# Kernel optimization log

Hardware: AMD Instinct MI355X
Metric: run time of the kernel (lower is better)

The kernel has to match this reference:

```python
import jax, jax.numpy as jnp
import numpy as np

N_NODES = 50000
N_EDGES = 800000
NODE_F = 128
EDGE_F = 64
HID = 128
N_LAYERS = 3
BN_EPS = 1e-5


def _bn(x, g, b):
    # BatchNorm1d in training mode: per-feature batch mean/var (biased)
    m = jnp.mean(x, axis=0)
    v = jnp.mean(jnp.square(x - m), axis=0)
    return g * (x - m) * jax.lax.rsqrt(v + BN_EPS) + b


def _gelu(x):
    return jax.nn.gelu(x, approximate=False)


def setup_inputs() -> dict:
    key = jax.random.key(0)
    ks = jax.random.split(key, 16)
    s_in = 1.0 / np.sqrt(NODE_F)
    s_h = 1.0 / np.sqrt(HID)
    s_2h = 1.0 / np.sqrt(2 * HID)
    s_e = 1.0 / np.sqrt(EDGE_F)
    L = N_LAYERS
    inp = {
        "x": jax.random.normal(ks[0], (N_NODES, NODE_F), jnp.float32),
        "edge_index": jax.random.randint(ks[1], (2, N_EDGES), 0, N_NODES, jnp.int64),
        "edge_attr": jax.random.normal(ks[2], (N_EDGES, EDGE_F), jnp.float32),
        # node_embed: Linear + BN
        "emb_w": jax.random.uniform(ks[3], (NODE_F, HID), jnp.float32, -s_in, s_in),
        "emb_b": jnp.zeros((HID,), jnp.float32),
        "emb_g": jnp.ones((HID,), jnp.float32),
        "emb_beta": jnp.zeros((HID,), jnp.float32),
        # per-layer GINEConv params (stacked over layers)
        "eps": jnp.zeros((L,), jnp.float32),
        "lin_e_w": jax.random.uniform(ks[4], (L, EDGE_F, HID), jnp.float32, -s_e, s_e),
        "lin_e_b": jnp.zeros((L, HID), jnp.float32),
        "w1": jax.random.uniform(ks[5], (L, HID, 2 * HID), jnp.float32, -s_h, s_h),
        "b1": jnp.zeros((L, 2 * HID), jnp.float32),
        "g1": jnp.ones((L, 2 * HID), jnp.float32),
        "beta1": jnp.zeros((L, 2 * HID), jnp.float32),
        "w2": jax.random.uniform(ks[6], (L, 2 * HID, HID), jnp.float32, -s_2h, s_2h),
        "b2": jnp.zeros((L, HID), jnp.float32),
        "g2": jnp.ones((L, HID), jnp.float32),
        "beta2": jnp.zeros((L, HID), jnp.float32),
    }
    return inp


def reference(x, edge_index, edge_attr, emb_w, emb_b, emb_g, emb_beta,
              eps, lin_e_w, lin_e_b, w1, b1, g1, beta1, w2, b2, g2, beta2):
    src = edge_index[0]  # source nodes j
    dst = edge_index[1]  # target nodes i
    n = x.shape[0]

    h = _gelu(_bn(x @ emb_w + emb_b, emb_g, emb_beta))  # [N, H]
    intermediates = [h]
    for i in range(N_LAYERS):
        e = edge_attr @ lin_e_w[i] + lin_e_b[i]          # [E, H]
        msg = jax.nn.relu(h[src] + e)                    # gather + fuse + relu
        agg = jax.ops.segment_sum(msg, dst, num_segments=n)  # scatter-add
        z = (1.0 + eps[i]) * h + agg
        z = _gelu(_bn(z @ w1[i] + b1[i], g1[i], beta1[i]))
        h = _gelu(_bn(z @ w2[i] + b2[i], g2[i], beta2[i]))
        intermediates.append(h)
    return jnp.concatenate(intermediates, axis=-1)  # [N, (L+1)*H]
```

## Files before the change

### kernel.cpp

```cpp
#include <hip/hip_runtime.h>
#include <hip/hip_bf16.h>

typedef __hip_bfloat16 bf16;
typedef __attribute__((ext_vector_type(8))) short bf16x8;
typedef __attribute__((ext_vector_type(4))) float f32x4;

#define HIDDEN 128
#define NNODES 50000
#define NEDGES 800000

static __device__ __forceinline__ float b2f(bf16 v) { return __bfloat162float(v); }
static __device__ __forceinline__ short f2bs(float f) {
    bf16 b = __float2bfloat16(f);
    return *reinterpret_cast<const short*>(&b);
}
static __device__ __forceinline__ float bs2f(short s) {
    unsigned x = ((unsigned)(unsigned short)s) << 16;
    return *reinterpret_cast<const float*>(&x);
}
static __device__ __forceinline__ bf16x8 ld_frag(const bf16* p) {
    return *reinterpret_cast<const bf16x8*>(p);
}
static __device__ __forceinline__ bf16x8 zero8() {
    bf16x8 z = {0, 0, 0, 0, 0, 0, 0, 0};
    return z;
}
static __device__ __forceinline__ float u2f_lo(unsigned u) {
    unsigned x = u << 16; return *reinterpret_cast<const float*>(&x);
}
static __device__ __forceinline__ float u2f_hi(unsigned u) {
    unsigned x = u & 0xffff0000u; return *reinterpret_cast<const float*>(&x);
}
static __device__ __forceinline__ bf16x8 ld_a8(const void* base, size_t off, bool f32) {
    if (!f32) return *reinterpret_cast<const bf16x8*>((const bf16*)base + off);
    const float4* p = reinterpret_cast<const float4*>((const float*)base + off);
    float4 u = p[0], w = p[1];
    bf16x8 r;
    r[0]=f2bs(u.x); r[1]=f2bs(u.y); r[2]=f2bs(u.z); r[3]=f2bs(u.w);
    r[4]=f2bs(w.x); r[5]=f2bs(w.y); r[6]=f2bs(w.z); r[7]=f2bs(w.w);
    return r;
}
static __device__ __forceinline__ float gelu_ex(float v) {
    return 0.5f * v * (1.f + erff(v * 0.70710678118654752f));
}

#define C_EMB_B   0
#define C_EMB_G   128
#define C_EMB_BT  256
#define C_EPS     384
#define C_LIN_B   400
#define C_B1      800
#define C_G1      1568
#define C_BT1     2336
#define C_B2      3104
#define C_G2      3488
#define C_BT2     3872

__global__ void k_init(float* __restrict__ stats, int* __restrict__ cursorA,
                       int* __restrict__ cursorB, int doSort) {
    int tid = blockIdx.x * 256 + threadIdx.x;
    int stride = gridDim.x * 256;
    for (int i = tid; i < 3584; i += stride) stats[i] = 0.f;
    if (doSort) for (int i = tid; i < NNODES; i += stride) cursorA[i] = 0;
    for (int i = tid; i < NNODES; i += stride) cursorB[i] = 0;
}

__global__ void k_detect_cvt(const unsigned* __restrict__ gones,
                             const unsigned* __restrict__ eiw, int* __restrict__ flags,
                             const void* emb_b, const void* emb_g, const void* emb_bt,
                             const void* eps, const void* lin_b, const void* b1,
                             const void* g1, const void* bt1, const void* b2,
                             const void* g2, const void* bt2, bf16* __restrict__ canon) {
    __shared__ int sf;
    if (threadIdx.x == 0) {
        int f0 = (gones[0] == 0x3F803F80u) ? 1 : 0;
        unsigned s = 0;
        for (int i = 1; i < 64; i += 2) s |= eiw[i];
        flags[0] = f0; flags[1] = (s == 0u) ? 1 : 0;
        sf = f0;
    }
    __syncthreads();
    bool f32 = (sf == 0);
    const void* ps[11] = {emb_b, emb_g, emb_bt, eps, lin_b, b1, g1, bt1, b2, g2, bt2};
    const int   ns[11] = {128, 128, 128, 3, 384, 768, 768, 768, 384, 384, 384};
    const int   os[11] = {C_EMB_B, C_EMB_G, C_EMB_BT, C_EPS, C_LIN_B, C_B1,
                          C_G1, C_BT1, C_B2, C_G2, C_BT2};
    for (int seg = 0; seg < 11; ++seg)
        for (int i = threadIdx.x; i < ns[seg]; i += 256) {
            short v = f32 ? f2bs(((const float*)ps[seg])[i]) : ((const short*)ps[seg])[i];
            ((short*)canon)[os[seg] + i] = v;
        }
}

__global__ void k_repack_all(const void* __restrict__ emb_w, const void* __restrict__ lin_w,
                             const void* __restrict__ w1, const void* __restrict__ w2,
                             bf16* __restrict__ Wf, const int* __restrict__ flags) {
    const int starts[11] = {0, 16384, 24576, 32768, 40960, 73728, 106496,
                            139264, 172032, 204800, 237568};
    int idx = blockIdx.x * 256 + threadIdx.x;
    if (idx >= 237568) return;
    bool f32 = (flags[0] == 0);
    int seg = 0;
    while (idx >= starts[seg + 1]) ++seg;
    int local = idx - starts[seg];
    const void* base; long long eoff; int K, N;
    if (seg == 0)      { base = emb_w; eoff = 0;                          K = 128; N = 128; }
    else if (seg <= 3) { base = lin_w; eoff = (long long)(seg - 1) * 8192;  K = 64;  N = 128; }
    else if (seg <= 6) { base = w1;    eoff = (long long)(seg - 4) * 32768; K = 128; N = 256; }
    else               { base = w2;    eoff = (long long)(seg - 7) * 32768; K = 256; N = 128; }
    int j    = local & 7;
    int lane = (local >> 3) & 63;
    int rest = local >> 9;
    int NF   = N >> 4;
    int ks   = rest / NF;
    int nf   = rest - ks * NF;
    int k = ks * 32 + ((lane >> 4) << 3) + j;
    int n = (nf << 4) + (lane & 15);
    long long src = eoff + (long long)k * N + n;
    short v = f32 ? f2bs(((const float*)base)[src]) : ((const short*)base)[src];
    ((short*)Wf)[idx] = v;
}

__global__ void k_hist(const void* __restrict__ ei, int* __restrict__ deg,
                       const int* __restrict__ flags) {
    bool i64 = (flags[1] == 1);
    for (int e = blockIdx.x * 256 + threadIdx.x; e < NEDGES; e += gridDim.x * 256) {
        int d = i64 ? (int)((const long long*)ei)[NEDGES + e] : ((const int*)ei)[NEDGES + e];
        if ((unsigned)d < NNODES) atomicAdd(&deg[d], 1);
    }
}

__global__ __launch_bounds__(1024) void k_scan(const int* __restrict__ deg,
                                               int* __restrict__ rowptr) {
    __shared__ int part[1024];
    const int CH = 49;
    int t = threadIdx.x;
    int lo = t * CH, hi = lo + CH; if (hi > NNODES) hi = NNODES; if (lo > NNODES) lo = NNODES;
    int s = 0;
    for (int i = lo; i < hi; ++i) s += deg[i];
    part[t] = s;
    __syncthreads();
    for (int off = 1; off < 1024; off <<= 1) {
        int v = (t >= off) ? part[t - off] : 0;
        __syncthreads();
        part[t] += v;
        __syncthreads();
    }
    int run = (t == 0) ? 0 : part[t - 1];
    for (int i = lo; i < hi; ++i) { rowptr[i] = run; run += deg[i]; }
    if (t == 1023) rowptr[NNODES] = run;
}

__global__ void k_scatter(const void* __restrict__ ei, const int* __restrict__ rowptr,
                          int* __restrict__ cursor, int* __restrict__ srcs,
                          int* __restrict__ dsts, int* __restrict__ eids,
                          int* __restrict__ pos_of,
                          const int* __restrict__ flags) {
    bool i64 = (flags[1] == 1);
    for (int e = blockIdx.x * 256 + threadIdx.x; e < NEDGES; e += gridDim.x * 256) {
        int s, d;
        if (i64) {
            s = (int)((const long long*)ei)[e];
            d = (int)((const long long*)ei)[NEDGES + e];
        } else {
            s = ((const int*)ei)[e];
            d = ((const int*)ei)[NEDGES + e];
        }
        if ((unsigned)s >= NNODES || (unsigned)d >= NNODES) { pos_of[e] = -1; continue; }
        int pos = rowptr[d] + atomicAdd(&cursor[d], 1);
        srcs[pos] = s; dsts[pos] = d; eids[pos] = e; pos_of[e] = pos;
    }
}

__global__ void k_permEA3(const void* __restrict__ EA, const int* __restrict__ pos_of,
                          bf16* __restrict__ eaP, const int* __restrict__ flags) {
    bool f32 = (flags[0] == 0);
    int tid = blockIdx.x * 256 + threadIdx.x;
    int t = tid & 7;
    int r0 = (tid >> 3) * 4;
    if (r0 >= NEDGES) return;
    int p[4];
#pragma unroll
    for (int j = 0; j < 4; ++j) p[j] = pos_of[r0 + j];
    if (f32) {
        float4 a[4], b[4];
#pragma unroll
        for (int j = 0; j < 4; ++j) {
            const float4* q = reinterpret_cast<const float4*>(
                (const float*)EA + (size_t)(r0 + j) * 64 + t * 8);
            a[j] = q[0]; b[j] = q[1];
        }
#pragma unroll
        for (int j = 0; j < 4; ++j) {
            if (p[j] < 0) continue;
            bf16x8 r;
            r[0]=f2bs(a[j].x); r[1]=f2bs(a[j].y); r[2]=f2bs(a[j].z); r[3]=f2bs(a[j].w);
            r[4]=f2bs(b[j].x); r[5]=f2bs(b[j].y); r[6]=f2bs(b[j].z); r[7]=f2bs(b[j].w);
            *reinterpret_cast<bf16x8*>(eaP + (size_t)p[j] * 64 + t * 8) = r;
        }
    } else {
        bf16x8 a[4];
#pragma unroll
        for (int j = 0; j < 4; ++j)
            a[j] = *reinterpret_cast<const bf16x8*>(
                (const bf16*)EA + (size_t)(r0 + j) * 64 + t * 8);
#pragma unroll
        for (int j = 0; j < 4; ++j) {
            if (p[j] < 0) continue;
            *reinterpret_cast<bf16x8*>(eaP + (size_t)p[j] * 64 + t * 8) = a[j];
        }
    }
}

template<int K, int NF>
__global__ __launch_bounds__(256) void k_gemm(const void* __restrict__ A,
                                              const bf16* __restrict__ Wf,
                                              const bf16* __restrict__ bias,
                                              bf16* __restrict__ Y, int M,
                                              float* __restrict__ ssum,
                                              float* __restrict__ ssq,
                                              const int* __restrict__ flags, int flexA) {
    const int N = NF * 16;
    __shared__ float sred[2][4][N];
    bool f32 = flexA && (flags[0] == 0);
    int lane = threadIdx.x & 63, wave = threadIdx.x >> 6;
    int rowbase = blockIdx.x * 64 + wave * 16;
    int arow = rowbase + (lane & 15);
    bool aval = (arow < M);
    size_t abase = (size_t)arow * K + ((lane >> 4) << 3);
    f32x4 acc[NF] = {};
#pragma unroll
    for (int ks = 0; ks < K / 32; ++ks) {
        bf16x8 a = aval ? ld_a8(A, abase + ks * 32, f32) : zero8();
#pragma unroll
        for (int f = 0; f < NF; ++f) {
            bf16x8 b = ld_frag(Wf + (((ks * NF + f) * 64 + lane) << 3));
            acc[f] = __builtin_amdgcn_mfma_f32_16x16x32_bf16(a, b, acc[f], 0, 0, 0);
        }
    }
    int hi = lane >> 4, coll = lane & 15;
    int crow = rowbase + hi * 4;
#pragma unroll
    for (int f = 0; f < NF; ++f) {
        int col = f * 16 + coll;
        float bv = b2f(bias[col]);
        float s = 0.f, q = 0.f;
#pragma unroll
        for (int r = 0; r < 4; ++r) {
            int row = crow + r;
            if (row < M) {
                float v = acc[f][r] + bv;
                Y[(size_t)row * N + col] = __float2bfloat16(v);
                s += v; q += v * v;
            }
        }
        s += __shfl_xor(s, 16); s += __shfl_xor(s, 32);
        q += __shfl_xor(q, 16); q += __shfl_xor(q, 32);
        if (hi == 0) { sred[0][wave][col] = s; sred[1][wave][col] = q; }
    }
    __syncthreads();
    for (int t = threadIdx.x; t < N; t += 256) {
        float s = sred[0][0][t] + sred[0][1][t] + sred[0][2][t] + sred[0][3][t];
        float q = sred[1][0][t] + sred[1][1][t] + sred[1][2][t] + sred[1][3][t];
        atomicAdd(&ssum[t], s); atomicAdd(&ssq[t], q);
    }
}

template<int NF>
__global__ __launch_bounds__(256) void k_gemm_zin(const bf16* __restrict__ h,
                                                  const float* __restrict__ agg,
                                                  const bf16* __restrict__ epsc, int layer,
                                                  const bf16* __restrict__ Wf,
                                                  const bf16* __restrict__ bias,
                                                  bf16* __restrict__ Y, int M,
                                                  float* __restrict__ ssum,
                                                  float* __restrict__ ssq) {
    const int K = 128, N = NF * 16;
    __shared__ float sred[2][4][N];
    float e1 = 1.f + b2f(epsc[layer]);
    int lane = threadIdx.x & 63, wave = threadIdx.x >> 6;
    int rowbase = blockIdx.x * 64 + wave * 16;
    int arow = rowbase + (lane & 15);
    bool aval = (arow < M);
    size_t abase = (size_t)arow * K + ((lane >> 4) << 3);
    f32x4 acc[NF] = {};
#pragma unroll
    for (int ks = 0; ks < 4; ++ks) {
        bf16x8 a;
        if (aval) {
            size_t off = abase + ks * 32;
            bf16x8 hv = ld_frag(h + off);
            float4 a0 = *reinterpret_cast<const float4*>(agg + off);
            float4 a1 = *reinterpret_cast<const float4*>(agg + off + 4);
            a[0] = f2bs(e1 * bs2f(hv[0]) + a0.x);
            a[1] = f2bs(e1 * bs2f(hv[1]) + a0.y);
            a[2] = f2bs(e1 * bs2f(hv[2]) + a0.z);
            a[3] = f2bs(e1 * bs2f(hv[3]) + a0.w);
            a[4] = f2bs(e1 * bs2f(hv[4]) + a1.x);
            a[5] = f2bs(e1 * bs2f(hv[5]) + a1.y);
            a[6] = f2bs(e1 * bs2f(hv[6]) + a1.z);
            a[7] = f2bs(e1 * bs2f(hv[7]) + a1.w);
        } else {
            a = zero8();
        }
#pragma unroll
        for (int f = 0; f < NF; ++f) {
            bf16x8 b = ld_frag(Wf + (((ks * NF + f) * 64 + lane) << 3));
            acc[f] = __builtin_amdgcn_mfma_f32_16x16x32_bf16(a, b, acc[f], 0, 0, 0);
        }
    }
    int hi = lane >> 4, coll = lane & 15;
    int crow = rowbase + hi * 4;
#pragma unroll
    for (int f = 0; f < NF; ++f) {
        int col = f * 16 + coll;
        float bv = b2f(bias[col]);
        float s = 0.f, q = 0.f;
#pragma unroll
        for (int r = 0; r < 4; ++r) {
            int row = crow + r;
            if (row < M) {
                float v = acc[f][r] + bv;
                Y[(size_t)row * N + col] = __float2bfloat16(v);
                s += v; q += v * v;
            }
        }
        s += __shfl_xor(s, 16); s += __shfl_xor(s, 32);
        q += __shfl_xor(q, 16); q += __shfl_xor(q, 32);
        if (hi == 0) { sred[0][wave][col] = s; sred[1][wave][col] = q; }
    }
    __syncthreads();
    for (int t = threadIdx.x; t < N; t += 256) {
        float s = sred[0][0][t] + sred[0][1][t] + sred[0][2][t] + sred[0][3][t];
        float q = sred[1][0][t] + sred[1][1][t] + sred[1][2][t] + sred[1][3][t];
        atomicAdd(&ssum[t], s); atomicAdd(&ssq[t], q);
    }
}

template<int NF>
__global__ __launch_bounds__(256) void k_gemm_bn(const bf16* __restrict__ A,
                                                 const float* __restrict__ ssumIn,
                                                 const float* __restrict__ ssqIn,
                                                 const bf16* __restrict__ gIn,
                                                 const bf16* __restrict__ btIn,
                                                 const bf16* __restrict__ Wf,
                                                 const bf16* __restrict__ bias,
                                                 bf16* __restrict__ Y, int M,
                                                 float* __restrict__ ssum,
                                                 float* __restrict__ ssq) {
    const int K = 256, N = NF * 16;
    __shared__ float sscale[K], sshift[K];
    __shared__ float sred[2][4][N];
    for (int c = threadIdx.x; c < K; c += 256) {
        const float invM = 1.f / (float)NNODES;
        float mean = ssumIn[c] * invM;
        float var  = ssqIn[c] * invM - mean * mean;
        float a = b2f(gIn[c]) * rsqrtf(fmaxf(var, 0.f) + 1e-5f);
        sscale[c] = a;
        sshift[c] = b2f(btIn[c]) - mean * a;
    }
    __syncthreads();
    int lane = threadIdx.x & 63, wave = threadIdx.x >> 6;
    int rowbase = blockIdx.x * 64 + wave * 16;
    int arow = rowbase + (lane & 15);
    bool aval = (arow < M);
    int koff = (lane >> 4) << 3;
    size_t abase = (size_t)arow * K + koff;
    f32x4 acc[NF] = {};
#pragma unroll
    for (int ks = 0; ks < 8; ++ks) {
        bf16x8 a;
        if (aval) {
            bf16x8 raw = ld_frag(A + abase + ks * 32);
            int c0 = ks * 32 + koff;
#pragma unroll
            for (int j = 0; j < 8; ++j) {
                float v = bs2f(raw[j]) * sscale[c0 + j] + sshift[c0 + j];
                a[j] = f2bs(gelu_ex(v));
            }
        } else {
            a = zero8();
        }
#pragma unroll
        for (int f = 0; f < NF; ++f) {
            bf16x8 b = ld_frag(Wf + (((ks * NF + f) * 64 + lane) << 3));
            acc[f] = __builtin_amdgcn_mfma_f32_16x16x32_bf16(a, b, acc[f], 0, 0, 0);
        }
    }
    int hi = lane >> 4, coll = lane & 15;
    int crow = rowbase + hi * 4;
#pragma unroll
    for (int f = 0; f < NF; ++f) {
        int col = f * 16 + coll;
        float bv = b2f(bias[col]);
        float s = 0.f, q = 0.f;
#pragma unroll
        for (int r = 0; r < 4; ++r) {
            int row = crow + r;
            if (row < M) {
                float v = acc[f][r] + bv;
                Y[(size_t)row * N + col] = __float2bfloat16(v);
                s += v; q += v * v;
            }
        }
        s += __shfl_xor(s, 16); s += __shfl_xor(s, 32);
        q += __shfl_xor(q, 16); q += __shfl_xor(q, 32);
        if (hi == 0) { sred[0][wave][col] = s; sred[1][wave][col] = q; }
    }
    __syncthreads();
    for (int t = threadIdx.x; t < N; t += 256) {
        float s = sred[0][0][t] + sred[0][1][t] + sred[0][2][t] + sred[0][3][t];
        float q = sred[1][0][t] + sred[1][1][t] + sred[1][2][t] + sred[1][3][t];
        atomicAdd(&ssum[t], s); atomicAdd(&ssq[t], q);
    }
}

__global__ __launch_bounds__(64) void k_edge5(const bf16* __restrict__ eaP,
                                              const void* __restrict__ EA,
                                              const int* __restrict__ eids,
                                              const bf16* __restrict__ Wf,
                                              const bf16* __restrict__ bias,
                                              const int* __restrict__ srcs,
                                              const int* __restrict__ dsts,
                                              const bf16* __restrict__ h,
                                              float* __restrict__ agg,
                                              const int* __restrict__ flags) {
    __shared__ short sm[16 * 132];
    bool f32 = (flags[0] == 0);
    int lane = threadIdx.x & 63;
    int base = blockIdx.x * 16;
    int arow = base + (lane & 15);
    int koff = (lane >> 4) << 3;
    int l2 = lane * 2;
    int idx16 = base + (lane & 15);
    int ss_l = srcs[idx16];
    int ds_l = dsts[idx16];
    int ok_l = ((unsigned)ss_l < NNODES && (unsigned)ds_l < NNODES) ? 1 : 0;
    int sc_l = ok_l ? ss_l : 0;
    f32x4 acc[8] = {};
    if (eaP) {
        const bf16* ap = eaP + (size_t)arow * 64 + koff;
#pragma unroll
        for (int ks = 0; ks < 2; ++ks) {
            bf16x8 a = ld_frag(ap + ks * 32);
#pragma unroll
            for (int f = 0; f < 8; ++f) {
                bf16x8 b = ld_frag(Wf + (((ks * 8 + f) * 64 + lane) << 3));
                acc[f] = __builtin_amdgcn_mfma_f32_16x16x32_bf16(a, b, acc[f], 0, 0, 0);
            }
        }
    } else {
        size_t abase = (size_t)eids[arow] * 64 + koff;
#pragma unroll
        for (int ks = 0; ks < 2; ++ks) {
            bf16x8 a = ld_a8(EA, abase + ks * 32, f32);
#pragma unroll
            for (int f = 0; f < 8; ++f) {
                bf16x8 b = ld_frag(Wf + (((ks * 8 + f) * 64 + lane) << 3));
                acc[f] = __builtin_amdgcn_mfma_f32_16x16x32_bf16(a, b, acc[f], 0, 0, 0);
            }
        }
    }
    unsigned hv[16];
#pragma unroll
    for (int e = 0; e < 16; ++e) {
        int s = __shfl(sc_l, e);
        hv[e] = *reinterpret_cast<const unsigned*>(
            reinterpret_cast<const unsigned short*>(h) + (size_t)s * 128 + l2);
    }
    int hi = lane >> 4, coll = lane & 15;
    int rbase = hi * 4;
#pragma unroll
    for (int f = 0; f < 8; ++f)
#pragma unroll
        for (int r = 0; r < 4; ++r)
            sm[(rbase + r) * 132 + f * 16 + coll] = f2bs(acc[f][r]);
    __syncthreads();
    float bx = b2f(bias[l2]), by = b2f(bias[l2 + 1]);
    float rx = 0.f, ry = 0.f;
    int rd = -1;
#pragma unroll
    for (int e = 0; e < 16; ++e) {
        int d  = __shfl(ds_l, e);
        int ok = __shfl(ok_l, e);
        if (!ok) continue;
        if (d != rd) {
            if (rd >= 0) {
                atomicAdd(&agg[(size_t)rd * 128 + l2], rx);
                atomicAdd(&agg[(size_t)rd * 128 + l2 + 1], ry);
            }
            rd = d; rx = 0.f; ry = 0.f;
        }
        unsigned mu = *reinterpret_cast<const unsigned*>(&sm[e * 132 + l2]);
        float vx = u2f_lo(mu) + u2f_lo(hv[e]) + bx;
        float vy = u2f_hi(mu) + u2f_hi(hv[e]) + by;
        rx += fmaxf(vx, 0.f); ry += fmaxf(vy, 0.f);
    }
    if (rd >= 0) {
        atomicAdd(&agg[(size_t)rd * 128 + l2], rx);
        atomicAdd(&agg[(size_t)rd * 128 + l2 + 1], ry);
    }
}

__global__ __launch_bounds__(256) void k_edge(const void* __restrict__ EA,
                                              const bf16* __restrict__ Wf,
                                              const bf16* __restrict__ bias,
                                              const void* __restrict__ ei,
                                              const bf16* __restrict__ h,
                                              float* __restrict__ agg,
                                              const int* __restrict__ flags) {
    bool f32 = (flags[0] == 0);
    bool i64 = (flags[1] == 1);
    const int K = 64, NF = 8;
    int lane = threadIdx.x & 63, wave = threadIdx.x >> 6;
    int rowbase = blockIdx.x * 64 + wave * 16;
    int colbase = blockIdx.y * 64;
    int arow = rowbase + (lane & 15);
    size_t abase = (size_t)arow * K + ((lane >> 4) << 3);
    f32x4 acc[4] = {};
#pragma unroll
    for (int ks = 0; ks < 2; ++ks) {
        bf16x8 a = ld_a8(EA, abase + ks * 32, f32);
#pragma unroll
        for (int f = 0; f < 4; ++f) {
            bf16x8 b = ld_frag(Wf + (((ks * NF + colbase / 16 + f) * 64 + lane) << 3));
            acc[f] = __builtin_amdgcn_mfma_f32_16x16x32_bf16(a, b, acc[f], 0, 0, 0);
        }
    }
    int erow = rowbase + ((lane >> 4) << 2);
    int coll = lane & 15;
    float bv[4];
#pragma unroll
    for (int f = 0; f < 4; ++f) bv[f] = b2f(bias[colbase + f * 16 + coll]);
#pragma unroll
    for (int r = 0; r < 4; ++r) {
        int e = erow + r;
        int s, d;
        if (i64) {
            s = (int)((const long long*)ei)[e];
            d = (int)((const long long*)ei)[NEDGES + e];
        } else {
            s = ((const int*)ei)[e];
            d = ((const int*)ei)[NEDGES + e];
        }
        if ((unsigned)s >= NNODES || (unsigned)d >= NNODES) continue;
        const bf16* hp = h + (size_t)s * HIDDEN;
        float* gp = agg + (size_t)d * HIDDEN;
#pragma unroll
        for (int f = 0; f < 4; ++f) {
            int col = colbase + f * 16 + coll;
            float v = acc[f][r] + bv[f] + b2f(hp[col]);
            if (v > 0.f) atomicAdd(gp + col, v);
        }
    }
}

template<int N>
__global__ void k_bngelu4(const bf16* __restrict__ y, const float* __restrict__ ssum,
                          const float* __restrict__ ssq, const bf16* __restrict__ g,
                          const bf16* __restrict__ beta, bf16* __restrict__ z,
                          void* __restrict__ out_base, int slice,
                          const int* __restrict__ flags,
                          float* __restrict__ aggz, int aggn4) {
    __shared__ float sscale[N], sshift[N];
    for (int c = threadIdx.x; c < N; c += 256) {
        const float invM = 1.f / (float)NNODES;
        float mean = ssum[c] * invM;
        float var  = ssq[c] * invM - mean * mean;
        float a = b2f(g[c]) * rsqrtf(fmaxf(var, 0.f) + 1e-5f);
        sscale[c] = a;
        sshift[c] = b2f(beta[c]) - mean * a;
    }
    __syncthreads();
    bool outb = (flags[0] == 1);
    const int total4 = NNODES * N / 4;
    for (int i4 = blockIdx.x * 256 + threadIdx.x; i4 < total4; i4 += gridDim.x * 256) {
        int i = i4 * 4;
        int col = i & (N - 1);
        ushort4 yv = ((const ushort4*)y)[i4];
        float g0 = gelu_ex(u2f_lo(yv.x) * sscale[col]     + sshift[col]);
        float g1 = gelu_ex(u2f_lo(yv.y) * sscale[col + 1] + sshift[col + 1]);
        float g2 = gelu_ex(u2f_lo(yv.z) * sscale[col + 2] + sshift[col + 2]);
        float g3 = gelu_ex(u2f_lo(yv.w) * sscale[col + 3] + sshift[col + 3]);
        ushort4 zv;
        zv.x = (unsigned short)f2bs(g0); zv.y = (unsigned short)f2bs(g1);
        zv.z = (unsigned short)f2bs(g2); zv.w = (unsigned short)f2bs(g3);
        ((ushort4*)z)[i4] = zv;
        if (slice >= 0) {
            int row = i / N;
            size_t ob = (size_t)row * 512 + (size_t)slice * 128 + col;
            if (outb) {
                *reinterpret_cast<ushort4*>((unsigned short*)out_base + ob) = zv;
            } else {
                float4 gv = {g0, g1, g2, g3};
                *reinterpret_cast<float4*>((float*)out_base + ob) = gv;
            }
        }
    }
    if (aggz) {
        float4 zzz = {0.f, 0.f, 0.f, 0.f};
        for (int i4 = blockIdx.x * 256 + threadIdx.x; i4 < aggn4; i4 += gridDim.x * 256)
            ((float4*)aggz)[i4] = zzz;
    }
}

extern "C" void kernel_launch(void* const* d_in, const int* in_sizes, int n_in,
                              void* d_out, int out_size, void* d_ws, size_t ws_size,
                              hipStream_t stream) {
    const void* x      = d_in[0];
    const void* ei     = d_in[1];
    const void* ea     = d_in[2];
    const void* emb_w  = d_in[3];
    const void* emb_b  = d_in[4];
    const void* emb_g  = d_in[5];
    const void* emb_bt = d_in[6];
    const void* eps    = d_in[7];
    const void* lin_w  = d_in[8];
    const void* lin_b  = d_in[9];
    const void* w1     = d_in[10];
    const void* b1     = d_in[11];
    const void* g1     = d_in[12];
    const void* bt1    = d_in[13];
    const void* w2     = d_in[14];
    const void* b2     = d_in[15];
    const void* g2     = d_in[16];
    const void* bt2    = d_in[17];

    char* ws = (char*)d_ws;
    int*   flags  = (int*)ws;
    float* stats  = (float*)(ws + 1024);
    bf16*  canon  = (bf16*)(ws + 16384);
    bf16*  wf0    = (bf16*)(ws + 32768);
    bf16*  lin_wf = wf0 + 16384;
    bf16*  w1f    = wf0 + 40960;
    bf16*  w2f    = wf0 + 139264;
    bf16*  bufH   = (bf16*)(ws + 524288);
    bf16*  bufA   = (bf16*)(ws + 13324288);
    char*  bufC   = (ws + 26124288);
    float* aggf   = (float*)bufC;
    bf16*  y1     = (bf16*)bufC;
    const size_t SB = 51724288;
    int*  rowptr  = (int*)(ws + SB);
    int*  cursorA = (int*)(ws + SB + 200704);
    int*  srcs    = (int*)(ws + SB + 401408);
    int*  dsts    = (int*)(ws + SB + 3601408);
    int*  eids    = (int*)(ws + SB + 6801408);
    bf16* eaP     = (bf16*)(ws + SB + 10001408);
    int*  cursorB = (int*)bufA;
    int*  pos_of  = (int*)(ws + 13324288 + 1048576);
    const unsigned long long TIERA_NEED = SB + 10001408ull + 102400000ull;
    const unsigned long long TIERB_NEED = SB + 10001408ull;
    bool tierA = ws_size >= TIERA_NEED;
    bool tierB = !tierA && ws_size >= TIERB_NEED;
    const int AGGN4 = NNODES * HIDDEN / 4;

    k_init<<<256, 256, 0, stream>>>(stats, cursorA, cursorB, (tierA || tierB) ? 1 : 0);
    k_detect_cvt<<<1, 256, 0, stream>>>((const unsigned*)emb_g, (const unsigned*)ei, flags,
                                        emb_b, emb_g, emb_bt, eps, lin_b, b1, g1, bt1,
                                        b2, g2, bt2, canon);
    k_repack_all<<<928, 256, 0, stream>>>(emb_w, lin_w, w1, w2, wf0, flags);

    if (tierA || tierB) {
        k_hist<<<1024, 256, 0, stream>>>(ei, cursorA, flags);
        k_scan<<<1, 1024, 0, stream>>>(cursorA, rowptr);
        k_scatter<<<1024, 256, 0, stream>>>(ei, rowptr, cursorB, srcs, dsts, eids,
                                            pos_of, flags);
        if (tierA) k_permEA3<<<6250, 256, 0, stream>>>(ea, pos_of, eaP, flags);
    }

    k_gemm<128, 8><<<782, 256, 0, stream>>>(x, wf0, canon + C_EMB_B, bufH, NNODES,
                                            stats, stats + 256, flags, 1);
    k_bngelu4<128><<<2048, 256, 0, stream>>>(bufH, stats, stats + 256,
                                             canon + C_EMB_G, canon + C_EMB_BT,
                                             bufH, d_out, 0, flags, aggf, AGGN4);

    for (int i = 0; i < 3; ++i) {
        float* s1 = stats + (size_t)(1 + 2 * i) * 512;
        float* s2 = stats + (size_t)(2 + 2 * i) * 512;
        if (tierA)
            k_edge5<<<50000, 64, 0, stream>>>(eaP, (const void*)nullptr, (const int*)nullptr,
                                              lin_wf + i * 8192, canon + C_LIN_B + i * 128,
                                              srcs, dsts, bufH, aggf, flags);
        else if (tierB)
            k_edge5<<<50000, 64, 0, stream>>>((const bf16*)nullptr, ea, eids,
                                              lin_wf + i * 8192, canon + C_LIN_B + i * 128,
                                              srcs, dsts, bufH, aggf, flags);
        else
            k_edge<<<dim3(12500, 2), 256, 0, stream>>>(ea, lin_wf + i * 8192,
                                                       canon + C_LIN_B + i * 128, ei,
                                                       bufH, aggf, flags);
        k_gemm_zin<16><<<782, 256, 0, stream>>>(bufH, aggf, canon + C_EPS, i,
                                                w1f + i * 32768, canon + C_B1 + i * 256,
                                                y1, NNODES, s1, s1 + 256);
        k_gemm_bn<8><<<782, 256, 0, stream>>>(y1, s1, s1 + 256, canon + C_G1 + i * 256,
                                              canon + C_BT1 + i * 256,
                                              w2f + i * 32768, canon + C_B2 + i * 128,
                                              bufA, NNODES, s2, s2 + 256);
        float* aggz = (i < 2) ? aggf : (float*)nullptr;
        k_bngelu4<128><<<2048, 256, 0, stream>>>(bufA, s2, s2 + 256, canon + C_G2 + i * 128,
                                                 canon + C_BT2 + i * 128, bufH, d_out,
                                                 i + 1, flags, aggz, AGGN4);
    }
}
```

Before: 1.013 ms.

## Switch edge kernel to one block per destination node with atomic-free writes

The edge message kernel now launches one 64-thread block per destination node and walks that node's CSR range of sorted edges in chunks of 16. Each node's sum is built in registers and written once, which removes the float atomics. Because every agg row is now fully overwritten, the separate zeroing of the aggregation buffer inside the BN/GELU kernel is skipped on the sorted path. In exchange, the ragged in-degree leaves lanes idle in partially filled chunks, and nodes with few edges still pay for a full 16-row MFMA tile plus per-block overhead.

```diff
diff --git a/kernel.cpp b/kernel.cpp
--- a/kernel.cpp
+++ b/kernel.cpp
@@ -415,91 +415,81 @@
     }
 }
 
-__global__ __launch_bounds__(64) void k_edge5(const bf16* __restrict__ eaP,
+__global__ __launch_bounds__(64) void k_edge6(const bf16* __restrict__ eaP,
                                               const void* __restrict__ EA,
                                               const int* __restrict__ eids,
                                               const bf16* __restrict__ Wf,
                                               const bf16* __restrict__ bias,
                                               const int* __restrict__ srcs,
-                                              const int* __restrict__ dsts,
+                                              const int* __restrict__ rowptr,
                                               const bf16* __restrict__ h,
                                               float* __restrict__ agg,
                                               const int* __restrict__ flags) {
     __shared__ short sm[16 * 132];
     bool f32 = (flags[0] == 0);
     int lane = threadIdx.x & 63;
-    int base = blockIdx.x * 16;
-    int arow = base + (lane & 15);
+    int d = blockIdx.x;
+    int start = rowptr[d], end = rowptr[d + 1];
     int koff = (lane >> 4) << 3;
     int l2 = lane * 2;
-    int idx16 = base + (lane & 15);
-    int ss_l = srcs[idx16];
-    int ds_l = dsts[idx16];
-    int ok_l = ((unsigned)ss_l < NNODES && (unsigned)ds_l < NNODES) ? 1 : 0;
-    int sc_l = ok_l ? ss_l : 0;
-    f32x4 acc[8] = {};
-    if (eaP) {
-        const bf16* ap = eaP + (size_t)arow * 64 + koff;
-#pragma unroll
-        for (int ks = 0; ks < 2; ++ks) {
-            bf16x8 a = ld_frag(ap + ks * 32);
-#pragma unroll
-            for (int f = 0; f < 8; ++f) {
-                bf16x8 b = ld_frag(Wf + (((ks * 8 + f) * 64 + lane) << 3));
-                acc[f] = __builtin_amdgcn_mfma_f32_16x16x32_bf16(a, b, acc[f], 0, 0, 0);
-            }
-        }
-    } else {
-        size_t abase = (size_t)eids[arow] * 64 + koff;
-#pragma unroll
-        for (int ks = 0; ks < 2; ++ks) {
-            bf16x8 a = ld_a8(EA, abase + ks * 32, f32);
-#pragma unroll
-            for (int f = 0; f < 8; ++f) {
-                bf16x8 b = ld_frag(Wf + (((ks * 8 + f) * 64 + lane) << 3));
-                acc[f] = __builtin_amdgcn_mfma_f32_16x16x32_bf16(a, b, acc[f], 0, 0, 0);
-            }
-        }
-    }
-    unsigned hv[16];
-#pragma unroll
-    for (int e = 0; e < 16; ++e) {
-        int s = __shfl(sc_l, e);
-        hv[e] = *reinterpret_cast<const unsigned*>(
-            reinterpret_cast<const unsigned short*>(h) + (size_t)s * 128 + l2);
-    }
     int hi = lane >> 4, coll = lane & 15;
     int rbase = hi * 4;
-#pragma unroll
-    for (int f = 0; f < 8; ++f)
-#pragma unroll
-        for (int r = 0; r < 4; ++r)
-            sm[(rbase + r) * 132 + f * 16 + coll] = f2bs(acc[f][r]);
-    __syncthreads();
     float bx = b2f(bias[l2]), by = b2f(bias[l2 + 1]);
     float rx = 0.f, ry = 0.f;
-    int rd = -1;
-#pragma unroll
-    for (int e = 0; e < 16; ++e) {
-        int d  = __shfl(ds_l, e);
-        int ok = __shfl(ok_l, e);
-        if (!ok) continue;
-        if (d != rd) {
-            if (rd >= 0) {
-                atomicAdd(&agg[(size_t)rd * 128 + l2], rx);
-                atomicAdd(&agg[(size_t)rd * 128 + l2 + 1], ry);
+    bool first = true;
+    for (int c = start; c < end; c += 16) {
+        int eidx = c + (lane & 15);
+        int ok_l = (eidx < end) ? 1 : 0;
+        int sc_l = ok_l ? srcs[eidx] : 0;
+        f32x4 acc[8] = {};
+        if (eaP) {
+            const bf16* ap = eaP + (size_t)eidx * 64 + koff;
+#pragma unroll
+            for (int ks = 0; ks < 2; ++ks) {
+                bf16x8 a = ok_l ? ld_frag(ap + ks * 32) : zero8();
+#pragma unroll
+                for (int f = 0; f < 8; ++f) {
+                    bf16x8 b = ld_frag(Wf + (((ks * 8 + f) * 64 + lane) << 3));
+                    acc[f] = __builtin_amdgcn_mfma_f32_16x16x32_bf16(a, b, acc[f], 0, 0, 0);
+                }
             }
-            rd = d; rx = 0.f; ry = 0.f;
-        }
-        unsigned mu = *reinterpret_cast<const unsigned*>(&sm[e * 132 + l2]);
-        float vx = u2f_lo(mu) + u2f_lo(hv[e]) + bx;
-        float vy = u2f_hi(mu) + u2f_hi(hv[e]) + by;
-        rx += fmaxf(vx, 0.f); ry += fmaxf(vy, 0.f);
-    }
-    if (rd >= 0) {
-        atomicAdd(&agg[(size_t)rd * 128 + l2], rx);
-        atomicAdd(&agg[(size_t)rd * 128 + l2 + 1], ry);
-    }
+        } else {
+            size_t abase = ok_l ? ((size_t)eids[eidx] * 64 + koff) : 0;
+#pragma unroll
+            for (int ks = 0; ks < 2; ++ks) {
+                bf16x8 a = ok_l ? ld_a8(EA, abase + ks * 32, f32) : zero8();
+#pragma unroll
+                for (int f = 0; f < 8; ++f) {
+                    bf16x8 b = ld_frag(Wf + (((ks * 8 + f) * 64 + lane) << 3));
+                    acc[f] = __builtin_amdgcn_mfma_f32_16x16x32_bf16(a, b, acc[f], 0, 0, 0);
+                }
+            }
+        }
+        unsigned hv[16];
+#pragma unroll
+        for (int e = 0; e < 16; ++e) {
+            int s = __shfl(sc_l, e);
+            hv[e] = *reinterpret_cast<const unsigned*>(
+                reinterpret_cast<const unsigned short*>(h) + (size_t)s * 128 + l2);
+        }
+        if (!first) __syncthreads();
+        first = false;
+#pragma unroll
+        for (int f = 0; f < 8; ++f)
+#pragma unroll
+            for (int r = 0; r < 4; ++r)
+                sm[(rbase + r) * 132 + f * 16 + coll] = f2bs(acc[f][r]);
+        __syncthreads();
+        int lim = end - c; if (lim > 16) lim = 16;
+        for (int e = 0; e < lim; ++e) {
+            unsigned mu = *reinterpret_cast<const unsigned*>(&sm[e * 132 + l2]);
+            float vx = u2f_lo(mu) + u2f_lo(hv[e]) + bx;
+            float vy = u2f_hi(mu) + u2f_hi(hv[e]) + by;
+            rx += fmaxf(vx, 0.f); ry += fmaxf(vy, 0.f);
+        }
+    }
+    agg[(size_t)d * 128 + l2]     = rx;
+    agg[(size_t)d * 128 + l2 + 1] = ry;
 }
 
 __global__ __launch_bounds__(256) void k_edge(const void* __restrict__ EA,
@@ -652,15 +642,16 @@
     const unsigned long long TIERB_NEED = SB + 10001408ull;
     bool tierA = ws_size >= TIERA_NEED;
     bool tierB = !tierA && ws_size >= TIERB_NEED;
+    bool sorted = tierA || tierB;
     const int AGGN4 = NNODES * HIDDEN / 4;
 
-    k_init<<<256, 256, 0, stream>>>(stats, cursorA, cursorB, (tierA || tierB) ? 1 : 0);
+    k_init<<<256, 256, 0, stream>>>(stats, cursorA, cursorB, sorted ? 1 : 0);
     k_detect_cvt<<<1, 256, 0, stream>>>((const unsigned*)emb_g, (const unsigned*)ei, flags,
                                         emb_b, emb_g, emb_bt, eps, lin_b, b1, g1, bt1,
                                         b2, g2, bt2, canon);
     k_repack_all<<<928, 256, 0, stream>>>(emb_w, lin_w, w1, w2, wf0, flags);
 
-    if (tierA || tierB) {
+    if (sorted) {
         k_hist<<<1024, 256, 0, stream>>>(ei, cursorA, flags);
         k_scan<<<1, 1024, 0, stream>>>(cursorA, rowptr);
         k_scatter<<<1024, 256, 0, stream>>>(ei, rowptr, cursorB, srcs, dsts, eids,
@@ -668,23 +659,24 @@
         if (tierA) k_permEA3<<<6250, 256, 0, stream>>>(ea, pos_of, eaP, flags);
     }
 
+    float* aggz0 = sorted ? (float*)nullptr : aggf;
     k_gemm<128, 8><<<782, 256, 0, stream>>>(x, wf0, canon + C_EMB_B, bufH, NNODES,
                                             stats, stats + 256, flags, 1);
     k_bngelu4<128><<<2048, 256, 0, stream>>>(bufH, stats, stats + 256,
                                              canon + C_EMB_G, canon + C_EMB_BT,
-                                             bufH, d_out, 0, flags, aggf, AGGN4);
+                                             bufH, d_out, 0, flags, aggz0, AGGN4);
 
     for (int i = 0; i < 3; ++i) {
         float* s1 = stats + (size_t)(1 + 2 * i) * 512;
         float* s2 = stats + (size_t)(2 + 2 * i) * 512;
         if (tierA)
-            k_edge5<<<50000, 64, 0, stream>>>(eaP, (const void*)nullptr, (const int*)nullptr,
-                                              lin_wf + i * 8192, canon + C_LIN_B + i * 128,
-                                              srcs, dsts, bufH, aggf, flags);
+            k_edge6<<<NNODES, 64, 0, stream>>>(eaP, (const void*)nullptr, (const int*)nullptr,
+                                               lin_wf + i * 8192, canon + C_LIN_B + i * 128,
+                                               srcs, rowptr, bufH, aggf, flags);
         else if (tierB)
-            k_edge5<<<50000, 64, 0, stream>>>((const bf16*)nullptr, ea, eids,
-                                              lin_wf + i * 8192, canon + C_LIN_B + i * 128,
-                                              srcs, dsts, bufH, aggf, flags);
+            k_edge6<<<NNODES, 64, 0, stream>>>((const bf16*)nullptr, ea, eids,
+                                               lin_wf + i * 8192, canon + C_LIN_B + i * 128,
+                                               srcs, rowptr, bufH, aggf, flags);
         else
             k_edge<<<dim3(12500, 2), 256, 0, stream>>>(ea, lin_wf + i * 8192,
                                                        canon + C_LIN_B + i * 128, ei,
@@ -696,7 +688,7 @@
                                               canon + C_BT1 + i * 256,
                                               w2f + i * 32768, canon + C_B2 + i * 128,
                                               bufA, NNODES, s2, s2 + 256);
-        float* aggz = (i < 2) ? aggf : (float*)nullptr;
+        float* aggz = (!sorted && i < 2) ? aggf : (float*)nullptr;
         k_bngelu4<128><<<2048, 256, 0, stream>>>(bufA, s2, s2 + 256, canon + C_G2 + i * 128,
                                                  canon + C_BT2 + i * 128, bufH, d_out,
                                                  i + 1, flags, aggz, AGGN4);
```

Result: faster. 926.0 us (-8.6%).
